# Kernel tuning notes

Measured on AMD Instinct MI355X. Metric: run time of the kernel, lower is better.

Reference implementation:

```python
import jax, jax.numpy as jnp
import numpy as np

N_NODES = 50000


def gcn_conv(x, W, b, src, dst, num_nodes):
    # GCNConv (PyG defaults): h = D^{-1/2} (A + I) D^{-1/2} x W + b
    h = x @ W  # [N, out_dim]
    deg = jax.ops.segment_sum(jnp.ones(src.shape[0], h.dtype), dst, num_segments=num_nodes)
    dinv = jnp.where(deg > 0, jax.lax.rsqrt(deg), 0.0)
    norm = dinv[src] * dinv[dst]  # [E]
    out = jax.ops.segment_sum(h[src] * norm[:, None], dst, num_segments=num_nodes)
    return out + b


def setup_inputs() -> dict:
    key = jax.random.key(0)
    k1, k2, k3, k4 = jax.random.split(key, 4)
    x = jax.random.normal(k1, (N_NODES, 512), dtype=jnp.float32)
    ei = jax.random.randint(k2, (2, 800000), 0, N_NODES, dtype=jnp.int64)
    # Glorot-like init for GCN linear weights; PyG bias init zeros
    W1 = jax.random.normal(k3, (512, 128), dtype=jnp.float32) * (1.0 / np.sqrt(512))
    b1 = jnp.zeros((128,), dtype=jnp.float32)
    W2 = jax.random.normal(k4, (128, 64), dtype=jnp.float32) * (1.0 / np.sqrt(128))
    b2 = jnp.zeros((64,), dtype=jnp.float32)
    return {"x": x, "ei": ei, "W1": W1, "b1": b1, "W2": W2, "b2": b2}


def reference(x, ei, W1, b1, W2, b2):
    n = x.shape[0]
    loops = jnp.arange(n, dtype=ei.dtype)
    src = jnp.concatenate([ei[0], loops])  # add self-loops (PyG default)
    dst = jnp.concatenate([ei[1], loops])
    h = jax.nn.relu(gcn_conv(x, W1, b1, src, dst, n))
    return jax.nn.relu(gcn_conv(h, W2, b2, src, dst, n))
```

## Files before the change

### kernel.cpp

```cpp
#include <hip/hip_runtime.h>


#define N_FEAT0 512
#define N_FEAT1 128
#define N_FEAT2 64
#define SLACK 64

typedef _Float16 f16x8 __attribute__((ext_vector_type(8)));
typedef float f32x16 __attribute__((ext_vector_type(16)));


__global__ void k_prep(const float* __restrict__ W1, const float* __restrict__ W2,
                       _Float16* __restrict__ Wt, _Float16* __restrict__ Wt2,
                       int* __restrict__ cnt, int n) {
    int idx = blockIdx.x * 256 + threadIdx.x;
    if (idx < 65536) {
        int k = idx >> 7;
        int c = idx & 127;
        Wt[(size_t)c * 512 + k] = (_Float16)W1[idx];
    } else if (idx < 65536 + 8192) {
        int j = idx - 65536;
        int k = j >> 6;
        int c = j & 63;
        Wt2[(size_t)c * 128 + k] = (_Float16)W2[j];
    }
    if (idx < n) cnt[idx] = 0;
}


__global__ void k_count_scatter(const int* __restrict__ src, const int* __restrict__ dst,
                                int* __restrict__ cnt, int* __restrict__ srcs_pad, int E) {
    const int t = blockIdx.x * blockDim.x + threadIdx.x;
    const int base = t * 4;
    if (base + 3 < E) {
        int4 d = *(const int4*)(dst + base);
        int4 s = *(const int4*)(src + base);
        int p0 = atomicAdd(&cnt[d.x], 1);
        int p1 = atomicAdd(&cnt[d.y], 1);
        int p2 = atomicAdd(&cnt[d.z], 1);
        int p3 = atomicAdd(&cnt[d.w], 1);
        if (p0 < SLACK) srcs_pad[(size_t)d.x * SLACK + p0] = s.x;
        if (p1 < SLACK) srcs_pad[(size_t)d.y * SLACK + p1] = s.y;
        if (p2 < SLACK) srcs_pad[(size_t)d.z * SLACK + p2] = s.z;
        if (p3 < SLACK) srcs_pad[(size_t)d.w * SLACK + p3] = s.w;
    } else {
        for (int i = base; i < E; i++) {
            int d = dst[i];
            int p = atomicAdd(&cnt[d], 1);
            if (p < SLACK) srcs_pad[(size_t)d * SLACK + p] = src[i];
        }
    }
}

__global__ __launch_bounds__(256) void k_gemm1_mfma(const float* __restrict__ X,
                                                    const _Float16* __restrict__ Wt,
                                                    const int* __restrict__ cnt,
                                                    _Float16* __restrict__ H, int n) {
    __shared__ __align__(16) _Float16 ah[4][32][8];
    __shared__ __align__(16) _Float16 wh[4][128][8];
    const int tid = threadIdx.x;
    const int lane = tid & 63;
    const int w = tid >> 6;
    const int row0 = blockIdx.x * 32;

    f32x16 acc0 = {};

    const int arow = tid >> 2;
    const int aoct = tid & 3;
    const bool ax = (tid < 128);
    const int gr = row0 + arow;
    const float* xrow = X + (size_t)gr * N_FEAT0 + aoct * 8;

    const int c0 = tid >> 2,          o0 = tid & 3;
    const int c1 = (tid + 256) >> 2,  o1 = tid & 3;
    const _Float16* wp0 = Wt + (size_t)c0 * 512 + o0 * 8;
    const _Float16* wp1 = Wt + (size_t)c1 * 512 + o1 * 8;

    float4 xa0, xb0, xa1, xb1;
    {
        const float4 z = make_float4(0.f, 0.f, 0.f, 0.f);
        if (ax && gr < n) {
            xa0 = ((const float4*)xrow)[0];
            xb0 = ((const float4*)xrow)[1];
            xa1 = ((const float4*)(xrow + 32))[0];
            xb1 = ((const float4*)(xrow + 32))[1];
        } else {
            xa0 = z; xb0 = z; xa1 = z; xb1 = z;
        }
    }
    f16x8 w0r = *(const f16x8*)wp0;
    f16x8 w1r = *(const f16x8*)wp1;

#define GCN_STEP(PA, PB, K0)                                                 \
    {                                                                        \
        if (ax) {                                                            \
            f16x8 hv;                                                        \
            hv[0] = (_Float16)PA.x; hv[1] = (_Float16)PA.y;                  \
            hv[2] = (_Float16)PA.z; hv[3] = (_Float16)PA.w;                  \
            hv[4] = (_Float16)PB.x; hv[5] = (_Float16)PB.y;                  \
            hv[6] = (_Float16)PB.z; hv[7] = (_Float16)PB.w;                  \
            *(f16x8*)(&ah[aoct][arow][0]) = hv;                              \
        }                                                                    \
        *(f16x8*)(&wh[o0][c0][0]) = w0r;                                     \
        *(f16x8*)(&wh[o1][c1][0]) = w1r;                                     \
        const int kx = (K0) + 64;                                            \
        if (kx < N_FEAT0 && ax && gr < n) {                                  \
            PA = ((const float4*)(xrow + kx))[0];                            \
            PB = ((const float4*)(xrow + kx))[1];                            \
        }                                                                    \
        const int kw = (K0) + 32;                                            \
        if (kw < N_FEAT0) {                                                  \
            w0r = *(const f16x8*)(wp0 + kw);                                 \
            w1r = *(const f16x8*)(wp1 + kw);                                 \
        }                                                                    \
        __syncthreads();                                                     \
        _Pragma("unroll")                                                    \
        for (int kb = 0; kb < 2; kb++) {                                     \
            const int oct = kb * 2 + (lane >> 5);                            \
            f16x8 a = *(const f16x8*)(&ah[oct][(lane & 31)][0]);             \
            f16x8 b = *(const f16x8*)(&wh[oct][w * 32 + (lane & 31)][0]);    \
            acc0 = __builtin_amdgcn_mfma_f32_32x32x16_f16(a, b, acc0, 0, 0, 0); \
        }                                                                    \
        __syncthreads();                                                     \
    }

    for (int t2 = 0; t2 < 8; t2++) {
        GCN_STEP(xa0, xb0, t2 * 64)
        GCN_STEP(xa1, xb1, t2 * 64 + 32)
    }
#undef GCN_STEP

    const int col = w * 32 + (lane & 31);
#pragma unroll
    for (int rq = 0; rq < 4; rq++)
#pragma unroll
        for (int rr = 0; rr < 4; rr++) {
            const int reg = rq * 4 + rr;
            const int row = row0 + rr + 8 * rq + 4 * (lane >> 5);
            if (row < n) {
                float di = rsqrtf((float)(cnt[row] + 1));
                H[(size_t)row * N_FEAT1 + col] = (_Float16)(acc0[reg] * di);
            }
        }
}

__global__ __launch_bounds__(256) void k_gemm2_mfma(const _Float16* __restrict__ A,
                                                    const _Float16* __restrict__ Wt2,
                                                    const int* __restrict__ cnt,
                                                    _Float16* __restrict__ H2, int n) {
    __shared__ __align__(16) _Float16 ah[16][128][8];
    __shared__ __align__(16) _Float16 bh[16][64][8];
    const int tid = threadIdx.x;
    const int lane = tid & 63;
    const int w = tid >> 6;
    const int row0 = blockIdx.x * 128;

#pragma unroll
    for (int it = 0; it < 8; it++) {
        int u = tid + it * 256;
        int r = u >> 4;
        int o = u & 15;
        int gr = row0 + r;
        f16x8 v = {};
        if (gr < n) v = *(const f16x8*)(A + (size_t)gr * 128 + o * 8);
        *(f16x8*)(&ah[o][r][0]) = v;
    }
#pragma unroll
    for (int it = 0; it < 4; it++) {
        int u = tid + it * 256;
        int c = u >> 4;
        int o = u & 15;
        *(f16x8*)(&bh[o][c][0]) = *(const f16x8*)(Wt2 + (size_t)c * 128 + o * 8);
    }
    __syncthreads();

    f32x16 acc0 = {}, acc1 = {};
#pragma unroll
    for (int s = 0; s < 8; s++) {
        const int oct = s * 2 + (lane >> 5);
        f16x8 a  = *(const f16x8*)(&ah[oct][w * 32 + (lane & 31)][0]);
        f16x8 b0 = *(const f16x8*)(&bh[oct][(lane & 31)][0]);
        f16x8 b1 = *(const f16x8*)(&bh[oct][32 + (lane & 31)][0]);
        acc0 = __builtin_amdgcn_mfma_f32_32x32x16_f16(a, b0, acc0, 0, 0, 0);
        acc1 = __builtin_amdgcn_mfma_f32_32x32x16_f16(a, b1, acc1, 0, 0, 0);
    }

#pragma unroll
    for (int rq = 0; rq < 4; rq++)
#pragma unroll
        for (int rr = 0; rr < 4; rr++) {
            const int row = row0 + w * 32 + rr + 8 * rq + 4 * (lane >> 5);
            if (row < n) {
                const float di = rsqrtf((float)(cnt[row] + 1));
                const int reg = rq * 4 + rr;
                H2[(size_t)row * N_FEAT2 + (lane & 31)] = (_Float16)(acc0[reg] * di);
                H2[(size_t)row * N_FEAT2 + 32 + (lane & 31)] = (_Float16)(acc1[reg] * di);
            }
        }
}


__global__ __launch_bounds__(256) void k_gather128(const int* __restrict__ srcs_pad,
                                                   const int* __restrict__ cnt,
                                                   const _Float16* __restrict__ H,
                                                   const float* __restrict__ bias,
                                                   _Float16* __restrict__ out, int n) {
    const int node = blockIdx.x * 16 + (threadIdx.x >> 4);
    const int li = threadIdx.x & 15;
    if (node >= n) return;
    const f16x8* __restrict__ H8 = (const f16x8*)H;
    f16x8 sv = H8[(size_t)node * 16 + li];
    float a[8];
#pragma unroll
    for (int q = 0; q < 8; q++) a[q] = (float)sv[q];
    const int c = cnt[node];
    const float di = rsqrtf((float)(c + 1));
    const int e = c < SLACK ? c : SLACK;
    const int* __restrict__ sp = srcs_pad + (size_t)node * SLACK;
    int j = 0;
    for (; j + 3 < e; j += 4) {
        int s0 = sp[j], s1 = sp[j + 1], s2 = sp[j + 2], s3 = sp[j + 3];
        f16x8 v0 = H8[(size_t)s0 * 16 + li];
        f16x8 v1 = H8[(size_t)s1 * 16 + li];
        f16x8 v2 = H8[(size_t)s2 * 16 + li];
        f16x8 v3 = H8[(size_t)s3 * 16 + li];
#pragma unroll
        for (int q = 0; q < 8; q++)
            a[q] += ((float)v0[q] + (float)v1[q]) + ((float)v2[q] + (float)v3[q]);
    }
    for (; j < e; j++) {
        f16x8 v0 = H8[(size_t)sp[j] * 16 + li];
#pragma unroll
        for (int q = 0; q < 8; q++) a[q] += (float)v0[q];
    }
    float4 b0 = *(const float4*)(bias + li * 8);
    float4 b1 = *(const float4*)(bias + li * 8 + 4);
    f16x8 r;
    r[0] = (_Float16)fmaxf(a[0] * di + b0.x, 0.f);
    r[1] = (_Float16)fmaxf(a[1] * di + b0.y, 0.f);
    r[2] = (_Float16)fmaxf(a[2] * di + b0.z, 0.f);
    r[3] = (_Float16)fmaxf(a[3] * di + b0.w, 0.f);
    r[4] = (_Float16)fmaxf(a[4] * di + b1.x, 0.f);
    r[5] = (_Float16)fmaxf(a[5] * di + b1.y, 0.f);
    r[6] = (_Float16)fmaxf(a[6] * di + b1.z, 0.f);
    r[7] = (_Float16)fmaxf(a[7] * di + b1.w, 0.f);
    ((f16x8*)out)[(size_t)node * 16 + li] = r;
}

__global__ __launch_bounds__(256) void k_gather64(const int* __restrict__ srcs_pad,
                                                  const int* __restrict__ cnt,
                                                  const _Float16* __restrict__ H,
                                                  const float* __restrict__ bias,
                                                  float* __restrict__ out, int n) {
    const int node = blockIdx.x * 32 + (threadIdx.x >> 3);
    const int li = threadIdx.x & 7;
    if (node >= n) return;
    const f16x8* __restrict__ H8 = (const f16x8*)H;
    f16x8 sv = H8[(size_t)node * 8 + li];
    float a[8];
#pragma unroll
    for (int q = 0; q < 8; q++) a[q] = (float)sv[q];
    const int c = cnt[node];
    const float di = rsqrtf((float)(c + 1));
    const int e = c < SLACK ? c : SLACK;
    const int* __restrict__ sp = srcs_pad + (size_t)node * SLACK;
    int j = 0;
    for (; j + 3 < e; j += 4) {
        int s0 = sp[j], s1 = sp[j + 1], s2 = sp[j + 2], s3 = sp[j + 3];
        f16x8 v0 = H8[(size_t)s0 * 8 + li];
        f16x8 v1 = H8[(size_t)s1 * 8 + li];
        f16x8 v2 = H8[(size_t)s2 * 8 + li];
        f16x8 v3 = H8[(size_t)s3 * 8 + li];
#pragma unroll
        for (int q = 0; q < 8; q++)
            a[q] += ((float)v0[q] + (float)v1[q]) + ((float)v2[q] + (float)v3[q]);
    }
    for (; j < e; j++) {
        f16x8 v0 = H8[(size_t)sp[j] * 8 + li];
#pragma unroll
        for (int q = 0; q < 8; q++) a[q] += (float)v0[q];
    }
    float4 b0 = *(const float4*)(bias + li * 8);
    float4 b1 = *(const float4*)(bias + li * 8 + 4);
    float4 r0, r1;
    r0.x = fmaxf(a[0] * di + b0.x, 0.f);
    r0.y = fmaxf(a[1] * di + b0.y, 0.f);
    r0.z = fmaxf(a[2] * di + b0.z, 0.f);
    r0.w = fmaxf(a[3] * di + b0.w, 0.f);
    r1.x = fmaxf(a[4] * di + b1.x, 0.f);
    r1.y = fmaxf(a[5] * di + b1.y, 0.f);
    r1.z = fmaxf(a[6] * di + b1.z, 0.f);
    r1.w = fmaxf(a[7] * di + b1.w, 0.f);
    float* op = out + (size_t)node * N_FEAT2 + li * 8;
    *(float4*)op = r0;
    *(float4*)(op + 4) = r1;
}


extern "C" void kernel_launch(void* const* d_in, const int* in_sizes, int n_in,
                              void* d_out, int out_size, void* d_ws, size_t ws_size,
                              hipStream_t stream) {
    const float* x  = (const float*)d_in[0];
    const int*   ei = (const int*)d_in[1];
    const float* W1 = (const float*)d_in[2];
    const float* b1 = (const float*)d_in[3];
    const float* W2 = (const float*)d_in[4];
    const float* b2 = (const float*)d_in[5];
    float* out = (float*)d_out;

    const int n = in_sizes[0] / N_FEAT0;
    const int E = in_sizes[1] / 2;
    const int* src = ei;
    const int* dst = ei + E;

    char* p = (char*)d_ws;
    _Float16* h16      = (_Float16*)p;
    _Float16* agg16    = (_Float16*)(p + 12800000);
    _Float16* h2_16    = (_Float16*)(p + 25600000);
    int*      cnt      = (int*)(p + 32000000);
    int*      srcs_pad = (int*)(p + 32200064);
    _Float16* Wt       = (_Float16*)(p + 45000064);
    _Float16* Wt2      = (_Float16*)(p + 45131136);

    const int B = 256;
    const int nprep = (65536 + 8192 > n ? 65536 + 8192 : n);

    k_prep<<<(nprep + B - 1) / B, B, 0, stream>>>(W1, W2, Wt, Wt2, cnt, n);
    k_count_scatter<<<((E + 3) / 4 + B - 1) / B, B, 0, stream>>>(src, dst, cnt, srcs_pad, E);

    k_gemm1_mfma<<<(n + 31) / 32, B, 0, stream>>>(x, Wt, cnt, h16, n);
    k_gather128<<<(n + 15) / 16, B, 0, stream>>>(srcs_pad, cnt, h16, b1, agg16, n);

    k_gemm2_mfma<<<(n + 127) / 128, B, 0, stream>>>(agg16, Wt2, cnt, h2_16, n);
    k_gather64<<<(n + 31) / 32, B, 0, stream>>>(srcs_pad, cnt, h2_16, b2, out, n);
}
```

Baseline: 146.0 us.

## Build padded adjacency via two-level bucket sort instead of global atomics

Replaces the single scatter kernel, which did per-edge global atomics into a per-node count array and scattered writes into padded source lists, with a bucketed counting sort. Edges are first histogrammed into 256-node buckets, prefix-scanned, and binned into a sorted array using shared-memory atomics. Each bucket is then built in LDS and written out to the padded lists with coalesced stores. This cuts contended global atomics and random writes, but adds four kernel launches, an extra 6.4MB round trip through the sorted buffer, and a 64KB LDS footprint per build block.

```diff
diff --git a/kernel.cpp b/kernel.cpp
--- a/kernel.cpp
+++ b/kernel.cpp
@@ -5,14 +5,17 @@
 #define N_FEAT1 128
 #define N_FEAT2 64
 #define SLACK 64
+#define BSH 8
+#define BSZ 256
 
 typedef _Float16 f16x8 __attribute__((ext_vector_type(8)));
 typedef float f32x16 __attribute__((ext_vector_type(16)));
+typedef unsigned long long u64;
 
 
 __global__ void k_prep(const float* __restrict__ W1, const float* __restrict__ W2,
                        _Float16* __restrict__ Wt, _Float16* __restrict__ Wt2,
-                       int* __restrict__ cnt, int n) {
+                       int* __restrict__ bucket_cnt) {
     int idx = blockIdx.x * 256 + threadIdx.x;
     if (idx < 65536) {
         int k = idx >> 7;
@@ -24,32 +27,123 @@
         int c = j & 63;
         Wt2[(size_t)c * 128 + k] = (_Float16)W2[j];
     }
-    if (idx < n) cnt[idx] = 0;
-}
-
-
-__global__ void k_count_scatter(const int* __restrict__ src, const int* __restrict__ dst,
-                                int* __restrict__ cnt, int* __restrict__ srcs_pad, int E) {
-    const int t = blockIdx.x * blockDim.x + threadIdx.x;
-    const int base = t * 4;
+    if (idx < 256) bucket_cnt[idx] = 0;
+}
+
+
+__global__ __launch_bounds__(256) void k_hist(const int* __restrict__ dst, int E,
+                                              int* __restrict__ bucket_cnt) {
+    __shared__ int lh[256];
+    const int tid = threadIdx.x;
+    lh[tid] = 0;
+    __syncthreads();
+    const int base = (blockIdx.x * 256 + tid) * 4;
     if (base + 3 < E) {
         int4 d = *(const int4*)(dst + base);
-        int4 s = *(const int4*)(src + base);
-        int p0 = atomicAdd(&cnt[d.x], 1);
-        int p1 = atomicAdd(&cnt[d.y], 1);
-        int p2 = atomicAdd(&cnt[d.z], 1);
-        int p3 = atomicAdd(&cnt[d.w], 1);
-        if (p0 < SLACK) srcs_pad[(size_t)d.x * SLACK + p0] = s.x;
-        if (p1 < SLACK) srcs_pad[(size_t)d.y * SLACK + p1] = s.y;
-        if (p2 < SLACK) srcs_pad[(size_t)d.z * SLACK + p2] = s.z;
-        if (p3 < SLACK) srcs_pad[(size_t)d.w * SLACK + p3] = s.w;
+        atomicAdd(&lh[d.x >> BSH], 1);
+        atomicAdd(&lh[d.y >> BSH], 1);
+        atomicAdd(&lh[d.z >> BSH], 1);
+        atomicAdd(&lh[d.w >> BSH], 1);
+    } else {
+        for (int i = base; i < E; i++) atomicAdd(&lh[dst[i] >> BSH], 1);
+    }
+    __syncthreads();
+    if (lh[tid] > 0) atomicAdd(&bucket_cnt[tid], lh[tid]);
+}
+
+
+__global__ __launch_bounds__(256) void k_scaninit(const int* __restrict__ bucket_cnt,
+                                                  int* __restrict__ cursor, int nb) {
+    __shared__ int ts[256];
+    const int tid = threadIdx.x;
+    int v = (tid < nb) ? bucket_cnt[tid] : 0;
+    ts[tid] = v;
+    __syncthreads();
+    for (int d = 1; d < 256; d <<= 1) {
+        int t = (tid >= d) ? ts[tid - d] : 0;
+        __syncthreads();
+        ts[tid] += t;
+        __syncthreads();
+    }
+    if (tid < nb) cursor[tid] = ts[tid] - v;
+}
+
+
+__global__ __launch_bounds__(256) void k_binscatter(const int* __restrict__ src,
+                                                    const int* __restrict__ dst,
+                                                    int* __restrict__ cursor,
+                                                    u64* __restrict__ sorted, int E) {
+    __shared__ int lh[256];
+    __shared__ int lbase[256];
+    const int tid = threadIdx.x;
+    lh[tid] = 0;
+    __syncthreads();
+    const int base = (blockIdx.x * 256 + tid) * 4;
+    const bool full = (base + 3 < E);
+    int4 d4, s4;
+    if (full) {
+        d4 = *(const int4*)(dst + base);
+        s4 = *(const int4*)(src + base);
+        atomicAdd(&lh[d4.x >> BSH], 1);
+        atomicAdd(&lh[d4.y >> BSH], 1);
+        atomicAdd(&lh[d4.z >> BSH], 1);
+        atomicAdd(&lh[d4.w >> BSH], 1);
+    } else {
+        for (int i = base; i < E; i++) atomicAdd(&lh[dst[i] >> BSH], 1);
+    }
+    __syncthreads();
+    lbase[tid] = (lh[tid] > 0) ? atomicAdd(&cursor[tid], lh[tid]) : 0;
+    lh[tid] = 0;
+    __syncthreads();
+    if (full) {
+        int b, r;
+        b = d4.x >> BSH; r = atomicAdd(&lh[b], 1);
+        sorted[lbase[b] + r] = ((u64)(unsigned)d4.x << 32) | (unsigned)s4.x;
+        b = d4.y >> BSH; r = atomicAdd(&lh[b], 1);
+        sorted[lbase[b] + r] = ((u64)(unsigned)d4.y << 32) | (unsigned)s4.y;
+        b = d4.z >> BSH; r = atomicAdd(&lh[b], 1);
+        sorted[lbase[b] + r] = ((u64)(unsigned)d4.z << 32) | (unsigned)s4.z;
+        b = d4.w >> BSH; r = atomicAdd(&lh[b], 1);
+        sorted[lbase[b] + r] = ((u64)(unsigned)d4.w << 32) | (unsigned)s4.w;
     } else {
         for (int i = base; i < E; i++) {
             int d = dst[i];
-            int p = atomicAdd(&cnt[d], 1);
-            if (p < SLACK) srcs_pad[(size_t)d * SLACK + p] = src[i];
+            int b = d >> BSH;
+            int r = atomicAdd(&lh[b], 1);
+            sorted[lbase[b] + r] = ((u64)(unsigned)d << 32) | (unsigned)src[i];
         }
     }
+}
+
+
+__global__ __launch_bounds__(256) void k_bucket_build(const u64* __restrict__ sorted,
+                                                      const int* __restrict__ bucket_cnt,
+                                                      const int* __restrict__ cursor,
+                                                      int* __restrict__ cnt,
+                                                      int* __restrict__ srcs_pad) {
+    __shared__ int lcnt[BSZ];
+    __shared__ int lsrc[BSZ * SLACK];
+    const int tid = threadIdx.x;
+    const int b = blockIdx.x;
+    lcnt[tid] = 0;
+    __syncthreads();
+    const int end = cursor[b];
+    const int start = end - bucket_cnt[b];
+    for (int i = start + tid; i < end; i += 256) {
+        u64 e = sorted[i];
+        int d = (int)(e >> 32);
+        int s = (int)(e & 0xffffffffu);
+        int ld = d & (BSZ - 1);
+        int p = atomicAdd(&lcnt[ld], 1);
+        if (p < SLACK) lsrc[ld * SLACK + p] = s;
+    }
+    __syncthreads();
+    cnt[b * BSZ + tid] = lcnt[tid];
+    int4* gp = (int4*)(srcs_pad + (size_t)b * BSZ * SLACK);
+    const int4* lp = (const int4*)lsrc;
+#pragma unroll
+    for (int k = 0; k < (BSZ * SLACK / 4) / 256; k++)
+        gp[tid + k * 256] = lp[tid + k * 256];
 }
 
 __global__ __launch_bounds__(256) void k_gemm1_mfma(const float* __restrict__ X,
@@ -312,21 +406,29 @@
     const int E = in_sizes[1] / 2;
     const int* src = ei;
     const int* dst = ei + E;
+    const int nb = (n + BSZ - 1) >> BSH;
 
     char* p = (char*)d_ws;
-    _Float16* h16      = (_Float16*)p;
-    _Float16* agg16    = (_Float16*)(p + 12800000);
-    _Float16* h2_16    = (_Float16*)(p + 25600000);
-    int*      cnt      = (int*)(p + 32000000);
-    int*      srcs_pad = (int*)(p + 32200064);
-    _Float16* Wt       = (_Float16*)(p + 45000064);
-    _Float16* Wt2      = (_Float16*)(p + 45131136);
+    _Float16* h16        = (_Float16*)p;
+    _Float16* agg16      = (_Float16*)(p + 12800000);
+    _Float16* h2_16      = (_Float16*)(p + 25600000);
+    int*      cnt        = (int*)(p + 32000000);
+    int*      srcs_pad   = (int*)(p + 32200704);
+    u64*      sorted     = (u64*)(p + 45045760);
+    _Float16* Wt         = (_Float16*)(p + 51445760);
+    _Float16* Wt2        = (_Float16*)(p + 51576832);
+    int*      bucket_cnt = (int*)(p + 51593216);
+    int*      cursor     = (int*)(p + 51594240);
 
     const int B = 256;
-    const int nprep = (65536 + 8192 > n ? 65536 + 8192 : n);
-
-    k_prep<<<(nprep + B - 1) / B, B, 0, stream>>>(W1, W2, Wt, Wt2, cnt, n);
-    k_count_scatter<<<((E + 3) / 4 + B - 1) / B, B, 0, stream>>>(src, dst, cnt, srcs_pad, E);
+    const int nprep = 65536 + 8192;
+    const int nebk = ((E + 3) / 4 + B - 1) / B;
+
+    k_prep<<<(nprep + B - 1) / B, B, 0, stream>>>(W1, W2, Wt, Wt2, bucket_cnt);
+    k_hist<<<nebk, B, 0, stream>>>(dst, E, bucket_cnt);
+    k_scaninit<<<1, B, 0, stream>>>(bucket_cnt, cursor, nb);
+    k_binscatter<<<nebk, B, 0, stream>>>(src, dst, cursor, sorted, E);
+    k_bucket_build<<<nb, B, 0, stream>>>(sorted, bucket_cnt, cursor, cnt, srcs_pad);
 
     k_gemm1_mfma<<<(n + 31) / 32, B, 0, stream>>>(x, Wt, cnt, h16, n);
     k_gather128<<<(n + 15) / 16, B, 0, stream>>>(srcs_pad, cnt, h16, b1, agg16, n);
```

Measured after the change: 143.9 us. Within noise of the previous version (-1.4%).
